# Performance work log

Hardware: AMD Instinct MI355X
Metric: run time of the kernel (lower is better)

The kernel has to match this reference:

```python
import jax, jax.numpy as jnp
import numpy as np

B, F, S, D = 8, 4, 512, 256
H, DK, DV = 8, 32, 32
LN_EPS = 1e-5


def setup_inputs() -> dict:
    key = jax.random.key(0)
    ks = jax.random.split(key, 8)
    scale = 1.0 / np.sqrt(D)
    return {
        "x": jax.random.normal(ks[0], (B, F, S, D), dtype=jnp.float32),
        "res_att": jax.random.normal(ks[1], (B, F, H, S, S), dtype=jnp.float32),
        # weights stored as [in, out] (transpose of torch Linear.weight)
        "W_Q": jax.random.normal(ks[2], (D, H * DK), dtype=jnp.float32) * scale,
        "W_K": jax.random.normal(ks[3], (D, H * DK), dtype=jnp.float32) * scale,
        "W_V": jax.random.normal(ks[4], (D, H * DV), dtype=jnp.float32) * scale,
        "W_fc": jax.random.normal(ks[5], (H * DV, D), dtype=jnp.float32) * scale,
        "ln_g": jnp.ones((D,), dtype=jnp.float32),
        "ln_b": jnp.zeros((D,), dtype=jnp.float32),
    }


def _layer_norm(x, g, b):
    mu = jnp.mean(x, axis=-1, keepdims=True)
    var = jnp.var(x, axis=-1, keepdims=True)
    return (x - mu) * jax.lax.rsqrt(var + LN_EPS) * g + b


def reference(x, res_att, W_Q, W_K, W_V, W_fc, ln_g, ln_b):
    # x: [B, F, S, D]; project and split heads -> [B, F, H, S, dk]
    q = (x @ W_Q).reshape(B, F, S, H, DK).transpose(0, 1, 3, 2, 4)
    k = (x @ W_K).reshape(B, F, S, H, DK).transpose(0, 1, 3, 2, 4)
    v = (x @ W_V).reshape(B, F, S, H, DV).transpose(0, 1, 3, 2, 4)
    # RealFormer-style residual attention bias
    scores = jnp.einsum("bfhsk,bfhtk->bfhst", q, k) / np.sqrt(DK) + res_att
    # NOTE: original uses F.softmax(scores, dim=3) -> over the QUERY axis
    attn = jax.nn.softmax(scores, axis=3)
    ctx = jnp.einsum("bfhst,bfhtv->bfhsv", attn, v)
    ctx = ctx.transpose(0, 1, 3, 2, 4).reshape(B, F, S, H * DV)
    out = ctx @ W_fc
    out = _layer_norm(out + x, ln_g, ln_b)
    return out, scores
```

## Files before the change

### kernel.cpp

```cpp
#include <hip/hip_runtime.h>
#include <math.h>

#define B_   8
#define F_   4
#define S_   512
#define D_   256
#define H_   8
#define DK_  32
#define DV_  32
#define NBF  32
#define NROWS (NBF * S_)
#define NG   (NBF * H_)
#define LN_EPS 1e-5f

typedef __attribute__((ext_vector_type(8))) short bf16x8;
typedef __attribute__((ext_vector_type(4))) float f32x4;
typedef __attribute__((ext_vector_type(8))) unsigned short u16x8;

__device__ __forceinline__ short f2bf(float f) {
    union { float f; unsigned u; } v; v.f = f;
    unsigned u = v.u;
    u += 0x7FFFu + ((u >> 16) & 1u);
    return (short)(u >> 16);
}

__device__ __forceinline__ bf16x8 pack8(float4 a, float4 b) {
    bf16x8 r;
    r[0] = f2bf(a.x); r[1] = f2bf(a.y); r[2] = f2bf(a.z); r[3] = f2bf(a.w);
    r[4] = f2bf(b.x); r[5] = f2bf(b.y); r[6] = f2bf(b.z); r[7] = f2bf(b.w);
    return r;
}

union BFU { u16x8 u; bf16x8 b; };

__global__ __launch_bounds__(64) void wpack_kernel(
    const float* __restrict__ Wq, const float* __restrict__ Wk,
    const float* __restrict__ Wv,
    unsigned short* __restrict__ Wp)
{
    const int bid  = blockIdx.x;
    const int ct   = bid & 15;
    const int ks   = (bid >> 4) & 7;
    const int wsel = bid >> 7;
    const float* W = (wsel == 0) ? Wq : (wsel == 1) ? Wk : Wv;
    const int lane = threadIdx.x;
    const int lr = lane & 15, lg = lane >> 4;
    u16x8 t;
#pragma unroll
    for (int j = 0; j < 8; ++j)
        t[j] = (unsigned short)f2bf(W[(ks * 32 + lg * 8 + j) * 256 + ct * 16 + lr]);
    *(u16x8*)(Wp + ((size_t)bid * 64 + lane) * 8) = t;
}

__global__ __launch_bounds__(256) void qkv_kernel(
    const float* __restrict__ x, const unsigned short* __restrict__ Wp,
    float* __restrict__ qo, float* __restrict__ ko, float* __restrict__ vo)
{
    const int bid    = blockIdx.x;
    const int rowblk = bid & 255;
    const int wsel   = bid >> 8;
    float* outp = (wsel == 0) ? qo : (wsel == 1) ? ko : vo;
    const int m0   = rowblk * 64;
    const int w    = threadIdx.x >> 6;
    const int lane = threadIdx.x & 63;
    const int lr = lane & 15, lg = lane >> 4;
    const int arow = m0 + w * 16 + lr;

    const f32x4 zero = {0.f, 0.f, 0.f, 0.f};
    f32x4 acc[16];
#pragma unroll
    for (int ct = 0; ct < 16; ++ct) acc[ct] = zero;

    for (int ks = 0; ks < 8; ++ks) {
        const float* xp = &x[(size_t)arow * 256 + ks * 32 + lg * 8];
        bf16x8 a = pack8(*(const float4*)xp, *(const float4*)(xp + 4));
        const u16x8* wp = (const u16x8*)(Wp + ((size_t)(wsel * 8 + ks) * 16) * 64 * 8);
#pragma unroll
        for (int ct = 0; ct < 16; ++ct) {
            BFU bb; bb.u = wp[ct * 64 + lane];
            acc[ct] = __builtin_amdgcn_mfma_f32_16x16x32_bf16(a, bb.b, acc[ct], 0, 0, 0);
        }
    }
#pragma unroll
    for (int ct = 0; ct < 16; ++ct)
#pragma unroll
        for (int j = 0; j < 4; ++j)
            outp[(size_t)(m0 + w * 16 + lg * 4 + j) * 256 + ct * 16 + lr] = acc[ct][j];
}

__global__ __launch_bounds__(512) void scores_kernel(
    const float* __restrict__ q, const float* __restrict__ k,
    const float* __restrict__ res, float* __restrict__ sc_out,
    float* __restrict__ pmax, float* __restrict__ psum)
{
    const int bid  = blockIdx.x;
    const int g    = bid & 255;
    const int stch = bid >> 8;
    const int st   = stch >> 1;
    const int ch   = stch & 1;
    const int bf = g >> 3, h = g & 7;
    const size_t qkbase = (size_t)bf * S_ * D_ + (size_t)h * 32;
    const size_t sbase  = (size_t)g * S_ * S_;
    const int s0 = st * 64, c0 = ch * 256;

    __shared__ float T[64][260];
    const int tid = threadIdx.x;

#pragma unroll
    for (int p = 0; p < 8; ++p) {
        int idx = tid + p * 512;
        int r = idx >> 6, c4 = (idx & 63) * 4;
        *(float4*)&T[r][c4] =
            *(const float4*)&res[sbase + (size_t)(s0 + r) * S_ + c0 + c4];
    }
    __syncthreads();

    const int w = tid >> 6, lane = tid & 63;
    const int lr = lane & 15, lg = lane >> 4;

    bf16x8 afrag[4];
#pragma unroll
    for (int rt = 0; rt < 4; ++rt) {
        const float* qp = &q[qkbase + (size_t)(s0 + rt * 16 + lr) * D_ + lg * 8];
        afrag[rt] = pack8(*(const float4*)qp, *(const float4*)(qp + 4));
    }

    const float scale = 0.17677669529663687f;
    const f32x4 zero = {0.f, 0.f, 0.f, 0.f};

#pragma unroll
    for (int ctl = 0; ctl < 2; ++ctl) {
        const int lcol = w * 32 + ctl * 16 + lr;
        const int tcol = c0 + lcol;
        const float* kp = &k[qkbase + (size_t)tcol * D_ + lg * 8];
        bf16x8 b = pack8(*(const float4*)kp, *(const float4*)(kp + 4));

        f32x4 accr[4];
#pragma unroll
        for (int rt = 0; rt < 4; ++rt)
            accr[rt] = __builtin_amdgcn_mfma_f32_16x16x32_bf16(afrag[rt], b, zero, 0, 0, 0);

        float sc[16];
#pragma unroll
        for (int rt = 0; rt < 4; ++rt)
#pragma unroll
            for (int j = 0; j < 4; ++j) {
                const int r = rt * 16 + lg * 4 + j;
                float v = fmaf(accr[rt][j], scale, T[r][lcol]);
                T[r][lcol] = v;
                sc[rt * 4 + j] = v;
            }
        float m = sc[0];
#pragma unroll
        for (int i = 1; i < 16; ++i) m = fmaxf(m, sc[i]);
        float z = 0.f;
#pragma unroll
        for (int i = 0; i < 16; ++i) z += __expf(sc[i] - m);
#pragma unroll
        for (int off = 16; off <= 32; off <<= 1) {
            float om = __shfl_xor(m, off);
            float oz = __shfl_xor(z, off);
            float nm = fmaxf(m, om);
            z = z * __expf(m - nm) + oz * __expf(om - nm);
            m = nm;
        }
        if (lg == 0) {
            pmax[((size_t)g * 8 + st) * S_ + tcol] = m;
            psum[((size_t)g * 8 + st) * S_ + tcol] = z;
        }
    }
    __syncthreads();

#pragma unroll
    for (int p = 0; p < 8; ++p) {
        int idx = tid + p * 512;
        int r = idx >> 6, c4 = (idx & 63) * 4;
        *(float4*)&sc_out[sbase + (size_t)(s0 + r) * S_ + c0 + c4] =
            *(float4*)&T[r][c4];
    }
}

__global__ __launch_bounds__(256) void stats_kernel(
    const float* __restrict__ pmax, const float* __restrict__ psum,
    float* __restrict__ M, float* __restrict__ iZ)
{
    const int idx = blockIdx.x * 256 + threadIdx.x;
    const int g = idx >> 9;
    const int t = idx & 511;
    float m = -1e30f;
    float pm[8];
#pragma unroll
    for (int i = 0; i < 8; ++i) {
        pm[i] = pmax[((size_t)g * 8 + i) * S_ + t];
        m = fmaxf(m, pm[i]);
    }
    float z = 0.f;
#pragma unroll
    for (int i = 0; i < 8; ++i)
        z += psum[((size_t)g * 8 + i) * S_ + t] * __expf(pm[i] - m);
    M[idx]  = m;
    iZ[idx] = 1.f / z;
}

__global__ __launch_bounds__(256) void pv_kernel(
    const float* __restrict__ sc, const float* __restrict__ v,
    const float* __restrict__ M, const float* __restrict__ iZ,
    float* __restrict__ ctx)
{
    const int bid = blockIdx.x;
    const int g   = bid & 255;
    const int rt  = 7 - (bid >> 8);
    const int bf = g >> 3, h = g & 7;
    const size_t sbase = (size_t)g * S_ * S_;

    __shared__ unsigned short VT[32][520];
    __shared__ float Ml[S_];
    __shared__ float iZl[S_];
    const int tid = threadIdx.x;

    for (int i = tid; i < S_; i += 256) {
        Ml[i]  = M[(size_t)g * S_ + i];
        iZl[i] = iZ[(size_t)g * S_ + i];
    }
    for (int i = tid; i < S_ * 8; i += 256) {
        int t = i >> 3, v4 = (i & 7) * 4;
        float4 vv = *(const float4*)&v[((size_t)bf * S_ + t) * D_ + h * 32 + v4];
        VT[v4 + 0][t] = (unsigned short)f2bf(vv.x);
        VT[v4 + 1][t] = (unsigned short)f2bf(vv.y);
        VT[v4 + 2][t] = (unsigned short)f2bf(vv.z);
        VT[v4 + 3][t] = (unsigned short)f2bf(vv.w);
    }
    __syncthreads();

    const int w = tid >> 6, lane = tid & 63;
    const int lr = lane & 15, lg = lane >> 4;
    const int srow = rt * 64 + w * 16 + lr;

    const f32x4 zero = {0.f, 0.f, 0.f, 0.f};
    f32x4 acc[2] = {zero, zero};

    for (int kt = 0; kt < 16; ++kt) {
        const int t0 = kt * 32 + lg * 8;
        const float* sp = &sc[sbase + (size_t)srow * S_ + t0];
        float4 sa = *(const float4*)sp;
        float4 sb = *(const float4*)(sp + 4);
        bf16x8 a;
        a[0] = f2bf(__expf(sa.x - Ml[t0 + 0]) * iZl[t0 + 0]);
        a[1] = f2bf(__expf(sa.y - Ml[t0 + 1]) * iZl[t0 + 1]);
        a[2] = f2bf(__expf(sa.z - Ml[t0 + 2]) * iZl[t0 + 2]);
        a[3] = f2bf(__expf(sa.w - Ml[t0 + 3]) * iZl[t0 + 3]);
        a[4] = f2bf(__expf(sb.x - Ml[t0 + 4]) * iZl[t0 + 4]);
        a[5] = f2bf(__expf(sb.y - Ml[t0 + 5]) * iZl[t0 + 5]);
        a[6] = f2bf(__expf(sb.z - Ml[t0 + 6]) * iZl[t0 + 6]);
        a[7] = f2bf(__expf(sb.w - Ml[t0 + 7]) * iZl[t0 + 7]);
#pragma unroll
        for (int ct = 0; ct < 2; ++ct) {
            BFU bb;
            bb.u = *(u16x8*)&VT[ct * 16 + lr][kt * 32 + lg * 8];
            acc[ct] = __builtin_amdgcn_mfma_f32_16x16x32_bf16(a, bb.b, acc[ct], 0, 0, 0);
        }
    }
#pragma unroll
    for (int ct = 0; ct < 2; ++ct)
#pragma unroll
        for (int j = 0; j < 4; ++j)
            ctx[((size_t)bf * S_ + rt * 64 + w * 16 + lg * 4 + j) * D_
                + h * 32 + ct * 16 + lr] = acc[ct][j];
}

__global__ __launch_bounds__(256) void out_kernel(
    const float* __restrict__ ctx, const float* __restrict__ x,
    const float* __restrict__ Wfc, const float* __restrict__ gam,
    const float* __restrict__ bet, float* __restrict__ out)
{
    const int TM = 16;
    __shared__ float cs[TM][D_];
    __shared__ float red[TM][4][2];
    const int r0 = blockIdx.x * TM;
    const int j  = threadIdx.x;

    for (int i = threadIdx.x; i < TM * D_ / 4; i += 256) {
        int r = i / (D_ / 4);
        int c = (i % (D_ / 4)) * 4;
        *(float4*)&cs[r][c] = *(const float4*)&ctx[(size_t)(r0 + r) * D_ + c];
    }
    __syncthreads();

    float y[TM];
#pragma unroll
    for (int r = 0; r < TM; ++r) y[r] = 0.f;

    for (int kk = 0; kk < D_; kk += 4) {
        float w0 = Wfc[(kk + 0) * D_ + j], w1 = Wfc[(kk + 1) * D_ + j];
        float w2 = Wfc[(kk + 2) * D_ + j], w3 = Wfc[(kk + 3) * D_ + j];
#pragma unroll
        for (int r = 0; r < TM; ++r) {
            float4 c4 = *(const float4*)&cs[r][kk];
            y[r] = fmaf(c4.x, w0, y[r]); y[r] = fmaf(c4.y, w1, y[r]);
            y[r] = fmaf(c4.z, w2, y[r]); y[r] = fmaf(c4.w, w3, y[r]);
        }
    }
#pragma unroll
    for (int r = 0; r < TM; ++r) y[r] += x[(size_t)(r0 + r) * D_ + j];

    const int lane = threadIdx.x & 63;
    const int w    = threadIdx.x >> 6;
#pragma unroll
    for (int r = 0; r < TM; ++r) {
        float s1 = y[r], s2 = y[r] * y[r];
        for (int off = 32; off; off >>= 1) {
            s1 += __shfl_xor(s1, off);
            s2 += __shfl_xor(s2, off);
        }
        if (lane == 0) { red[r][w][0] = s1; red[r][w][1] = s2; }
    }
    __syncthreads();

#pragma unroll
    for (int r = 0; r < TM; ++r) {
        float s1 = red[r][0][0] + red[r][1][0] + red[r][2][0] + red[r][3][0];
        float s2 = red[r][0][1] + red[r][1][1] + red[r][2][1] + red[r][3][1];
        float mu  = s1 * (1.f / D_);
        float var = s2 * (1.f / D_) - mu * mu;
        float o = (y[r] - mu) * rsqrtf(var + LN_EPS) * gam[j] + bet[j];
        out[(size_t)(r0 + r) * D_ + j] = o;
    }
}

extern "C" void kernel_launch(void* const* d_in, const int* in_sizes, int n_in,
                              void* d_out, int out_size, void* d_ws, size_t ws_size,
                              hipStream_t stream)
{
    const float* x   = (const float*)d_in[0];
    const float* res = (const float*)d_in[1];
    const float* Wq  = (const float*)d_in[2];
    const float* Wk  = (const float*)d_in[3];
    const float* Wv  = (const float*)d_in[4];
    const float* Wfc = (const float*)d_in[5];
    const float* gam = (const float*)d_in[6];
    const float* bet = (const float*)d_in[7];

    float* out    = (float*)d_out;
    float* scores = out + (size_t)NROWS * D_;

    float* q    = (float*)d_ws;
    float* k    = q    + (size_t)NROWS * D_;
    float* v    = k    + (size_t)NROWS * D_;
    float* ctx  = v    + (size_t)NROWS * D_;
    float* pmax = ctx  + (size_t)NROWS * D_;
    float* psum = pmax + (size_t)NG * 8 * S_;
    float* M    = psum + (size_t)NG * 8 * S_;
    float* iZ   = M    + (size_t)NG * S_;
    unsigned short* Wp = (unsigned short*)ctx;

    wpack_kernel<<<dim3(384), 64, 0, stream>>>(Wq, Wk, Wv, Wp);
    qkv_kernel<<<dim3(768), 256, 0, stream>>>(x, Wp, q, k, v);
    scores_kernel<<<dim3(4096), 512, 0, stream>>>(q, k, res, scores, pmax, psum);
    stats_kernel<<<dim3(NG * S_ / 256), 256, 0, stream>>>(pmax, psum, M, iZ);
    pv_kernel<<<dim3(2048), 256, 0, stream>>>(scores, v, M, iZ, ctx);
    out_kernel<<<dim3(NROWS / 16), 256, 0, stream>>>(ctx, x, Wfc, gam, bet, out);
}
```

Measured before the change: 299.6 us.

## Move output projection to bf16 MFMA kernel and split out layernorm

```diff
diff --git a/kernel.cpp b/kernel.cpp
--- a/kernel.cpp
+++ b/kernel.cpp
@@ -35,14 +35,14 @@
 
 __global__ __launch_bounds__(64) void wpack_kernel(
     const float* __restrict__ Wq, const float* __restrict__ Wk,
-    const float* __restrict__ Wv,
+    const float* __restrict__ Wv, const float* __restrict__ Wfc,
     unsigned short* __restrict__ Wp)
 {
     const int bid  = blockIdx.x;
     const int ct   = bid & 15;
     const int ks   = (bid >> 4) & 7;
     const int wsel = bid >> 7;
-    const float* W = (wsel == 0) ? Wq : (wsel == 1) ? Wk : Wv;
+    const float* W = (wsel == 0) ? Wq : (wsel == 1) ? Wk : (wsel == 2) ? Wv : Wfc;
     const int lane = threadIdx.x;
     const int lr = lane & 15, lg = lane >> 4;
     u16x8 t;
@@ -268,43 +268,56 @@
                 + h * 32 + ct * 16 + lr] = acc[ct][j];
 }
 
-__global__ __launch_bounds__(256) void out_kernel(
-    const float* __restrict__ ctx, const float* __restrict__ x,
-    const float* __restrict__ Wfc, const float* __restrict__ gam,
-    const float* __restrict__ bet, float* __restrict__ out)
+__global__ __launch_bounds__(256) void fc_kernel(
+    const float* __restrict__ ctx, const unsigned short* __restrict__ Wp,
+    float* __restrict__ fc)
+{
+    const int rowblk = blockIdx.x;
+    const int m0   = rowblk * 64;
+    const int w    = threadIdx.x >> 6;
+    const int lane = threadIdx.x & 63;
+    const int lr = lane & 15, lg = lane >> 4;
+    const int arow = m0 + w * 16 + lr;
+
+    const f32x4 zero = {0.f, 0.f, 0.f, 0.f};
+    f32x4 acc[16];
+#pragma unroll
+    for (int ct = 0; ct < 16; ++ct) acc[ct] = zero;
+
+    for (int ks = 0; ks < 8; ++ks) {
+        const float* xp = &ctx[(size_t)arow * 256 + ks * 32 + lg * 8];
+        bf16x8 a = pack8(*(const float4*)xp, *(const float4*)(xp + 4));
+        const u16x8* wp = (const u16x8*)(Wp + ((size_t)(3 * 8 + ks) * 16) * 64 * 8);
+#pragma unroll
+        for (int ct = 0; ct < 16; ++ct) {
+            BFU bb; bb.u = wp[ct * 64 + lane];
+            acc[ct] = __builtin_amdgcn_mfma_f32_16x16x32_bf16(a, bb.b, acc[ct], 0, 0, 0);
+        }
+    }
+#pragma unroll
+    for (int ct = 0; ct < 16; ++ct)
+#pragma unroll
+        for (int j = 0; j < 4; ++j)
+            fc[(size_t)(m0 + w * 16 + lg * 4 + j) * 256 + ct * 16 + lr] = acc[ct][j];
+}
+
+__global__ __launch_bounds__(256) void ln_kernel(
+    const float* __restrict__ fc, const float* __restrict__ x,
+    const float* __restrict__ gam, const float* __restrict__ bet,
+    float* __restrict__ out)
 {
     const int TM = 16;
-    __shared__ float cs[TM][D_];
     __shared__ float red[TM][4][2];
     const int r0 = blockIdx.x * TM;
     const int j  = threadIdx.x;
-
-    for (int i = threadIdx.x; i < TM * D_ / 4; i += 256) {
-        int r = i / (D_ / 4);
-        int c = (i % (D_ / 4)) * 4;
-        *(float4*)&cs[r][c] = *(const float4*)&ctx[(size_t)(r0 + r) * D_ + c];
-    }
-    __syncthreads();
-
-    float y[TM];
-#pragma unroll
-    for (int r = 0; r < TM; ++r) y[r] = 0.f;
-
-    for (int kk = 0; kk < D_; kk += 4) {
-        float w0 = Wfc[(kk + 0) * D_ + j], w1 = Wfc[(kk + 1) * D_ + j];
-        float w2 = Wfc[(kk + 2) * D_ + j], w3 = Wfc[(kk + 3) * D_ + j];
-#pragma unroll
-        for (int r = 0; r < TM; ++r) {
-            float4 c4 = *(const float4*)&cs[r][kk];
-            y[r] = fmaf(c4.x, w0, y[r]); y[r] = fmaf(c4.y, w1, y[r]);
-            y[r] = fmaf(c4.z, w2, y[r]); y[r] = fmaf(c4.w, w3, y[r]);
-        }
-    }
-#pragma unroll
-    for (int r = 0; r < TM; ++r) y[r] += x[(size_t)(r0 + r) * D_ + j];
-
     const int lane = threadIdx.x & 63;
     const int w    = threadIdx.x >> 6;
+
+    float y[TM];
+#pragma unroll
+    for (int r = 0; r < TM; ++r)
+        y[r] = fc[(size_t)(r0 + r) * D_ + j] + x[(size_t)(r0 + r) * D_ + j];
+
 #pragma unroll
     for (int r = 0; r < TM; ++r) {
         float s1 = y[r], s2 = y[r] * y[r];
@@ -351,12 +364,14 @@
     float* psum = pmax + (size_t)NG * 8 * S_;
     float* M    = psum + (size_t)NG * 8 * S_;
     float* iZ   = M    + (size_t)NG * S_;
-    unsigned short* Wp = (unsigned short*)ctx;
-
-    wpack_kernel<<<dim3(384), 64, 0, stream>>>(Wq, Wk, Wv, Wp);
+    unsigned short* Wp = (unsigned short*)(iZ + (size_t)NG * S_);
+    float* fc   = (float*)(Wp + (size_t)512 * 64 * 8);
+
+    wpack_kernel<<<dim3(512), 64, 0, stream>>>(Wq, Wk, Wv, Wfc, Wp);
     qkv_kernel<<<dim3(768), 256, 0, stream>>>(x, Wp, q, k, v);
     scores_kernel<<<dim3(4096), 512, 0, stream>>>(q, k, res, scores, pmax, psum);
     stats_kernel<<<dim3(NG * S_ / 256), 256, 0, stream>>>(pmax, psum, M, iZ);
     pv_kernel<<<dim3(2048), 256, 0, stream>>>(scores, v, M, iZ, ctx);
-    out_kernel<<<dim3(NROWS / 16), 256, 0, stream>>>(ctx, x, Wfc, gam, bet, out);
-}
+    fc_kernel<<<dim3(256), 256, 0, stream>>>(ctx, Wp, fc);
+    ln_kernel<<<dim3(NROWS / 16), 256, 0, stream>>>(fc, x, gam, bet, out);
+}
```

Result: slower. 312.2 us (+4.2%).
